# Kernel optimization log

Measured on AMD Instinct MI355X. Metric: run time of the kernel, lower is better.

Reference implementation:

```python
import jax, jax.numpy as jnp
import numpy as np

D = 2048
N = 16384
E = 8
THRESHOLD = 0.5


def setup_inputs() -> dict:
    key = jax.random.key(0)
    ks = jax.random.split(key, 6)
    x = jax.random.normal(ks[0], (N, D), dtype=jnp.float32)
    # pretrained weight + truncated SVD basis (frozen in original module)
    W_np = np.asarray(jax.random.normal(ks[1], (D, D), dtype=jnp.float32))
    U, S, Vt = np.linalg.svd(W_np, full_matrices=False)
    k = int((np.cumsum(S) < THRESHOLD * S.sum()).sum())  # energy-threshold rank
    U_k = jnp.asarray(U[:, :k])
    V_k = jnp.asarray(Vt.T[:, :k])  # torch.svd returns V, not V^T
    W = jnp.asarray(W_np)
    lambda_k = jax.random.normal(ks[2], (E, k), dtype=jnp.float32)
    v = jnp.zeros((D,), dtype=jnp.float32)
    W_g1 = jax.random.normal(ks[3], (k, 1), dtype=jnp.float32)
    W_g2 = jax.random.normal(ks[4], (1, E), dtype=jnp.float32)
    return {"x": x, "W": W, "U_k": U_k, "V_k": V_k, "lambda_k": lambda_k,
            "v": v, "W_g1": W_g1, "W_g2": W_g2}


def reference(x, W, U_k, V_k, lambda_k, v, W_g1, W_g2):
    # Routing: g = softmax((x @ U_k) @ W_g1 @ W_g2)  -> [N, E]
    xu = x @ U_k                                   # [N, k] (shared with delta path)
    g = jax.nn.softmax((xu @ W_g1) @ W_g2, axis=-1)
    # sum_i g_i * (x @ (W + U diag(lam_i) V^T))
    #   = (x@W) * sum_i g_i  +  ((x@U) * (g @ lam)) @ V^T   (low-rank factored)
    base = x @ W                                   # [N, D], computed once
    coef = g @ lambda_k                            # [N, k]
    out = base * jnp.sum(g, axis=-1, keepdims=True) + (xu * coef) @ V_k.T
    return out * (1.0 + v)
```

## Files before the change

kernel.cpp:

```cpp
#include <hip/hip_runtime.h>
#include <hip/hip_bf16.h>

#define D_DIM 2048
#define E_DIM 8

typedef __attribute__((ext_vector_type(8))) short short8;
typedef __attribute__((ext_vector_type(4))) float f32x4;

__device__ __forceinline__ unsigned short f2bf(float f) {
  union { float f; unsigned int u; } v; v.f = f;
  unsigned int u = v.u;
  u += 0x7FFFu + ((u >> 16) & 1u);
  return (unsigned short)(u >> 16);
}

__device__ __forceinline__ void async_copy16(const void* g, void* l) {
  __builtin_amdgcn_global_load_lds((const __attribute__((address_space(1))) void*)g,
                                   (__attribute__((address_space(3))) void*)l,
                                   16, 0, 0);
}

__global__ void k_cvt_bf16(const float* __restrict__ in,
                           unsigned short* __restrict__ out, long long n) {
  long long i = ((long long)blockIdx.x * blockDim.x + threadIdx.x) * 8;
  const long long stride = (long long)gridDim.x * blockDim.x * 8;
  for (; i < n; i += stride) {
    float4 a = *(const float4*)(in + i);
    float4 b = *(const float4*)(in + i + 4);
    short8 r;
    r[0] = (short)f2bf(a.x); r[1] = (short)f2bf(a.y);
    r[2] = (short)f2bf(a.z); r[3] = (short)f2bf(a.w);
    r[4] = (short)f2bf(b.x); r[5] = (short)f2bf(b.y);
    r[6] = (short)f2bf(b.z); r[7] = (short)f2bf(b.w);
    *(short8*)(out + i) = r;
  }
}

__global__ void k_transpose_bf16(const float* __restrict__ in, int in_rows, int in_cols,
                                 int in_ld, unsigned short* __restrict__ out, int out_rows) {
  __shared__ float tile[32][33];
  const int tx = threadIdx.x;
  const int ty = threadIdx.y;
  const int c = blockIdx.x * 32 + tx;
  #pragma unroll
  for (int i = 0; i < 4; ++i) {
    const int r = blockIdx.y * 32 + ty + i * 8;
    float vv = 0.0f;
    if (r < in_rows && c < in_cols) vv = in[(size_t)r * in_ld + c];
    tile[ty + i * 8][tx] = vv;
  }
  __syncthreads();
  const int oc = blockIdx.y * 32 + tx;
  #pragma unroll
  for (int i = 0; i < 4; ++i) {
    const int orow = blockIdx.x * 32 + ty + i * 8;
    if (orow < out_rows && oc < in_rows)
      out[(size_t)orow * in_rows + oc] = f2bf(tile[tx][ty + i * 8]);
  }
}

__global__ void k_pad_bf16(const float* __restrict__ in, unsigned short* __restrict__ out,
                           int rows, int cols, int cols_pad) {
  long long idx = (long long)blockIdx.x * blockDim.x + threadIdx.x;
  const long long total = (long long)rows * cols_pad;
  const long long stride = (long long)gridDim.x * blockDim.x;
  for (; idx < total; idx += stride) {
    const int r = (int)(idx / cols_pad);
    const int c = (int)(idx % cols_pad);
    out[idx] = (c < cols) ? f2bf(in[(size_t)r * cols + c]) : (unsigned short)0;
  }
}

__global__ void k_route(const float* __restrict__ xu, int k, int k_pad,
                        const float* __restrict__ Wg1, const float* __restrict__ Wg2,
                        const float* __restrict__ lam,
                        unsigned short* __restrict__ A2, float* __restrict__ rowscale,
                        int Nrows) {
  const int w = threadIdx.x >> 6;
  const int lane = threadIdx.x & 63;
  const int row = blockIdx.x * 4 + w;
  if (row >= Nrows) return;
  const float* xr = xu + (size_t)row * k_pad;
  float s = 0.0f;
  for (int kk = lane; kk < k; kk += 64) s += xr[kk] * Wg1[kk];
  #pragma unroll
  for (int off = 32; off; off >>= 1) s += __shfl_xor(s, off);
  float lg[E_DIM];
  float mx = -INFINITY;
  #pragma unroll
  for (int e = 0; e < E_DIM; ++e) { lg[e] = s * Wg2[e]; mx = fmaxf(mx, lg[e]); }
  float Z = 0.0f;
  #pragma unroll
  for (int e = 0; e < E_DIM; ++e) { lg[e] = expf(lg[e] - mx); Z += lg[e]; }
  float g[E_DIM]; float gsum = 0.0f;
  #pragma unroll
  for (int e = 0; e < E_DIM; ++e) { g[e] = lg[e] / Z; gsum += g[e]; }
  const float inv = 1.0f / gsum;
  if (lane == 0) rowscale[row] = gsum;
  unsigned short* arow = A2 + (size_t)row * k_pad;
  for (int kk = lane; kk < k_pad; kk += 64) {
    if (kk < k) {
      float c = 0.0f;
      #pragma unroll
      for (int e = 0; e < E_DIM; ++e) c += g[e] * lam[(size_t)e * k + kk];
      arow[kk] = f2bf(xr[kk] * (c * inv));
    } else {
      arow[kk] = 0;
    }
  }
}

__global__ __launch_bounds__(256, 2) void k_gemm128(
    const unsigned short* __restrict__ A, long long lda,
    const unsigned short* __restrict__ B, long long ldb,
    int Ktot, float* __restrict__ Cout, int ldc) {
  __shared__ unsigned short lds[4 * 8192];
  const int tid = threadIdx.x;
  const int lane = tid & 63;
  const int w = tid >> 6;
  const long long brow = (long long)blockIdx.x * 128;
  const long long bcol = (long long)blockIdx.y * 128;
  const int c0 = w * 2;
  const int sr0 = lane >> 2;
  const int sj  = lane & 3;
  const int l15 = lane & 15;
  const int jhi = lane >> 4;
  const int wr = (w >> 1) * 64;
  const int wc = (w & 1) * 64;

  auto stage = [&](int tt) {
    unsigned short* dstA = lds + (tt & 3) * 8192;
    #pragma unroll
    for (int c = 0; c < 2; ++c) {
      const int chunk = c0 + c;
      const int lrow = chunk * 16 + sr0;
      const int jj = sj ^ ((lrow >> 1) & 3);
      async_copy16(A + (brow + lrow) * lda + (long long)tt * 32 + jj * 8,
                   (void*)(dstA + chunk * 512));
      async_copy16(B + (bcol + lrow) * ldb + (long long)tt * 32 + jj * 8,
                   (void*)(dstA + 4096 + chunk * 512));
    }
  };

  auto load_frags = [&](int tt, short8* av, short8* bv) {
    const unsigned short* Areg = lds + (tt & 3) * 8192;
    const unsigned short* Breg = Areg + 4096;
    #pragma unroll
    for (int m = 0; m < 4; ++m) {
      const int row = wr + m * 16 + l15;
      const int jj = jhi ^ ((row >> 1) & 3);
      av[m] = *(const short8*)(Areg + row * 32 + jj * 8);
    }
    #pragma unroll
    for (int n = 0; n < 4; ++n) {
      const int row = wc + n * 16 + l15;
      const int jj = jhi ^ ((row >> 1) & 3);
      bv[n] = *(const short8*)(Breg + row * 32 + jj * 8);
    }
  };

  f32x4 acc[4][4];
  #pragma unroll
  for (int m = 0; m < 4; ++m)
    #pragma unroll
    for (int n = 0; n < 4; ++n)
      #pragma unroll
      for (int j = 0; j < 4; ++j) acc[m][n][j] = 0.0f;

  auto do_mfma = [&](short8* av, short8* bv) {
    __builtin_amdgcn_s_setprio(1);
    #pragma unroll
    for (int m = 0; m < 4; ++m)
      #pragma unroll
      for (int n = 0; n < 4; ++n)
        acc[m][n] = __builtin_amdgcn_mfma_f32_16x16x32_bf16(av[m], bv[n], acc[m][n], 0, 0, 0);
    __builtin_amdgcn_s_setprio(0);
  };

  const int NT = Ktot >> 5;
  stage(0); stage(1); stage(2);
  asm volatile("s_waitcnt vmcnt(4)" ::: "memory");
  __builtin_amdgcn_s_barrier();

  short8 avA[4], bvA[4], avB[4], bvB[4];
  load_frags(0, avA, bvA);

  for (int t = 0; t < NT; t += 2) {
    if (t + 3 < NT) stage(t + 3);
    load_frags(t + 1, avB, bvB);
    do_mfma(avA, bvA);
    asm volatile("s_waitcnt vmcnt(4)" ::: "memory");
    __builtin_amdgcn_s_barrier();
    if (t + 4 < NT) stage(t + 4);
    if (t + 2 < NT) load_frags(t + 2, avA, bvA);
    do_mfma(avB, bvB);
    asm volatile("s_waitcnt vmcnt(4)" ::: "memory");
    __builtin_amdgcn_s_barrier();
  }

  #pragma unroll
  for (int m = 0; m < 4; ++m) {
    #pragma unroll
    for (int n = 0; n < 4; ++n) {
      const long long col = bcol + wc + n * 16 + l15;
      #pragma unroll
      for (int j = 0; j < 4; ++j) {
        const long long row = brow + wr + m * 16 + jhi * 4 + j;
        Cout[row * ldc + col] = acc[m][n][j];
      }
    }
  }
}

template<int EPI>
__global__ __launch_bounds__(512, 2) void k_gemm256(
    const unsigned short* __restrict__ A0, int lda0,
    const unsigned short* __restrict__ A1, int lda1,
    const unsigned short* __restrict__ B0, int ldb0,
    const unsigned short* __restrict__ B1, int ldb1,
    int ka0, int Ktot, int gridM,
    float* __restrict__ Cout, int ldc,
    const float* __restrict__ rowscale, const float* __restrict__ vcol) {
  __shared__ unsigned short lds[4 * 16384];
  const int tid = threadIdx.x;
  const int lane = tid & 63;
  const int w = tid >> 6;
  const int wm = w >> 2;
  const int wn = w & 3;

  int bid = blockIdx.x;
  const int cpx = gridDim.x >> 3;
  bid = (bid & 7) * cpx + (bid >> 3);
  const int bx = bid % gridM;
  const int by = bid / gridM;
  const long long brow = (long long)bx * 256;
  const long long bcol = (long long)by * 256;

  const int c0 = w * 2;
  const int sr0 = lane >> 2;
  const int sj  = lane & 3;
  const int l15 = lane & 15;
  const int jhi = lane >> 4;

  auto stage = [&](int tt) {
    const int k0 = tt * 32;
    const unsigned short* PA; long long ldA; long long kA;
    const unsigned short* PB; long long ldB; long long kB;
    if (k0 < ka0) { PA = A0; ldA = lda0; kA = k0;       PB = B0; ldB = ldb0; kB = k0; }
    else          { PA = A1; ldA = lda1; kA = k0 - ka0; PB = B1; ldB = ldb1; kB = k0 - ka0; }
    unsigned short* dst = lds + (tt & 3) * 16384;
    #pragma unroll
    for (int c = 0; c < 2; ++c) {
      const int chunk = c0 + c;
      const int lrow = chunk * 16 + sr0;
      const int jj = sj ^ ((lrow >> 1) & 3);
      async_copy16(PA + (brow + lrow) * ldA + kA + jj * 8, (void*)(dst + chunk * 512));
      async_copy16(PB + (bcol + lrow) * ldB + kB + jj * 8, (void*)(dst + 8192 + chunk * 512));
    }
  };

  auto load_frags = [&](int tt, short8* av, short8* bv) {
    const unsigned short* Areg = lds + (tt & 3) * 16384;
    const unsigned short* Breg = Areg + 8192;
    #pragma unroll
    for (int m = 0; m < 8; ++m) {
      const int row = wm * 128 + m * 16 + l15;
      const int jj = jhi ^ ((row >> 1) & 3);
      av[m] = *(const short8*)(Areg + row * 32 + jj * 8);
    }
    #pragma unroll
    for (int n = 0; n < 4; ++n) {
      const int row = wn * 64 + n * 16 + l15;
      const int jj = jhi ^ ((row >> 1) & 3);
      bv[n] = *(const short8*)(Breg + row * 32 + jj * 8);
    }
  };

  f32x4 acc[8][4];
  #pragma unroll
  for (int m = 0; m < 8; ++m)
    #pragma unroll
    for (int n = 0; n < 4; ++n)
      #pragma unroll
      for (int j = 0; j < 4; ++j) acc[m][n][j] = 0.0f;

  auto do_mfma = [&](short8* av, short8* bv) {
    __builtin_amdgcn_s_setprio(1);
    #pragma unroll
    for (int m = 0; m < 8; ++m)
      #pragma unroll
      for (int n = 0; n < 4; ++n)
        acc[m][n] = __builtin_amdgcn_mfma_f32_16x16x32_bf16(av[m], bv[n], acc[m][n], 0, 0, 0);
    __builtin_amdgcn_s_setprio(0);
  };

  const int NT = Ktot >> 5;
  stage(0); stage(1); stage(2);
  asm volatile("s_waitcnt vmcnt(4)" ::: "memory");
  __builtin_amdgcn_s_barrier();

  short8 avA[8], bvA[4], avB[8], bvB[4];
  load_frags(0, avA, bvA);

  for (int t = 0; t < NT; t += 2) {
    if (t + 3 < NT) stage(t + 3);
    load_frags(t + 1, avB, bvB);
    do_mfma(avA, bvA);
    asm volatile("s_waitcnt vmcnt(4)" ::: "memory");
    __builtin_amdgcn_s_barrier();
    if (t + 4 < NT) stage(t + 4);
    if (t + 2 < NT) load_frags(t + 2, avA, bvA);
    do_mfma(avB, bvB);
    asm volatile("s_waitcnt vmcnt(4)" ::: "memory");
    __builtin_amdgcn_s_barrier();
  }

  #pragma unroll
  for (int m = 0; m < 8; ++m) {
    #pragma unroll
    for (int n = 0; n < 4; ++n) {
      const long long col = bcol + wn * 64 + n * 16 + l15;
      float cs = 1.0f;
      if (EPI == 1) cs = 1.0f + vcol[col];
      #pragma unroll
      for (int j = 0; j < 4; ++j) {
        const long long row = brow + wm * 128 + m * 16 + jhi * 4 + j;
        float val = acc[m][n][j];
        if (EPI == 1) val *= rowscale[row] * cs;
        Cout[row * ldc + col] = val;
      }
    }
  }
}

extern "C" void kernel_launch(void* const* d_in, const int* in_sizes, int n_in,
                              void* d_out, int out_size, void* d_ws, size_t ws_size,
                              hipStream_t stream) {
  const float* x   = (const float*)d_in[0];
  const float* W   = (const float*)d_in[1];
  const float* U   = (const float*)d_in[2];
  const float* V   = (const float*)d_in[3];
  const float* lam = (const float*)d_in[4];
  const float* v   = (const float*)d_in[5];
  const float* Wg1 = (const float*)d_in[6];
  const float* Wg2 = (const float*)d_in[7];
  float* out = (float*)d_out;

  const int N = in_sizes[0] / D_DIM;
  const int k = in_sizes[2] / D_DIM;
  const int k_pad = (k + 127) & ~127;

  char* ws = (char*)d_ws;
  size_t off = 0;
  auto alloc = [&](size_t bytes) -> void* {
    void* p = ws + off;
    off += (bytes + 255) & ~(size_t)255;
    return p;
  };
  unsigned short* xb  = (unsigned short*)alloc((size_t)N * D_DIM * 2);
  unsigned short* Wt  = (unsigned short*)alloc((size_t)D_DIM * D_DIM * 2);
  unsigned short* Ukt = (unsigned short*)alloc((size_t)k_pad * D_DIM * 2);
  unsigned short* Vb  = (unsigned short*)alloc((size_t)D_DIM * k_pad * 2);
  float*          xu  = (float*)alloc((size_t)N * k_pad * 4);
  unsigned short* A2  = (unsigned short*)alloc((size_t)N * k_pad * 2);
  float*          rs  = (float*)alloc((size_t)N * 4);
  if (off > ws_size) return;

  k_cvt_bf16<<<2048, 256, 0, stream>>>(x, xb, (long long)N * D_DIM);
  k_transpose_bf16<<<dim3(D_DIM / 32, D_DIM / 32), dim3(32, 8), 0, stream>>>(
      W, D_DIM, D_DIM, D_DIM, Wt, D_DIM);
  k_transpose_bf16<<<dim3(k_pad / 32, D_DIM / 32), dim3(32, 8), 0, stream>>>(
      U, D_DIM, k, k, Ukt, k_pad);
  k_pad_bf16<<<512, 256, 0, stream>>>(V, Vb, D_DIM, k, k_pad);

  k_gemm128<<<dim3(N / 128, k_pad / 128), 256, 0, stream>>>(
      xb, D_DIM, Ukt, D_DIM, D_DIM, xu, k_pad);

  k_route<<<N / 4, 256, 0, stream>>>(xu, k, k_pad, Wg1, Wg2, lam, A2, rs, N);

  const int gridM = N / 256;
  const int gridN = D_DIM / 256;
  k_gemm256<1><<<gridM * gridN, 512, 0, stream>>>(
      xb, D_DIM, A2, k_pad,
      Wt, D_DIM, Vb, k_pad,
      D_DIM, D_DIM + k_pad, gridM,
      out, D_DIM, rs, v);
}
```

Before: 344.4 us.

## Restructure GEMM main loop into split-phase A/B staging with per-half MFMA

Splits the global-to-LDS staging into separate A and B halves and interleaves them with two half-tile MFMA phases per K step, replacing the double-buffered register fragments with a single smaller set. This cuts register pressure and is meant to overlap memory issue with compute more finely, following a ping-pong style schedule. In exchange it adds extra barriers per iteration and tail-dependent vmcnt waits, which may serialize waves and risks correctness if the wait counts do not match the outstanding loads.

```diff
diff --git a/kernel.cpp b/kernel.cpp
--- a/kernel.cpp
+++ b/kernel.cpp
@@ -242,12 +242,11 @@
   const int l15 = lane & 15;
   const int jhi = lane >> 4;
 
-  auto stage = [&](int tt) {
+  auto stageA = [&](int tt) {
     const int k0 = tt * 32;
     const unsigned short* PA; long long ldA; long long kA;
-    const unsigned short* PB; long long ldB; long long kB;
-    if (k0 < ka0) { PA = A0; ldA = lda0; kA = k0;       PB = B0; ldB = ldb0; kB = k0; }
-    else          { PA = A1; ldA = lda1; kA = k0 - ka0; PB = B1; ldB = ldb1; kB = k0 - ka0; }
+    if (k0 < ka0) { PA = A0; ldA = lda0; kA = k0; }
+    else          { PA = A1; ldA = lda1; kA = k0 - ka0; }
     unsigned short* dst = lds + (tt & 3) * 16384;
     #pragma unroll
     for (int c = 0; c < 2; ++c) {
@@ -255,15 +254,43 @@
       const int lrow = chunk * 16 + sr0;
       const int jj = sj ^ ((lrow >> 1) & 3);
       async_copy16(PA + (brow + lrow) * ldA + kA + jj * 8, (void*)(dst + chunk * 512));
-      async_copy16(PB + (bcol + lrow) * ldB + kB + jj * 8, (void*)(dst + 8192 + chunk * 512));
-    }
-  };
-
-  auto load_frags = [&](int tt, short8* av, short8* bv) {
-    const unsigned short* Areg = lds + (tt & 3) * 16384;
+    }
+  };
+  auto stageB = [&](int tt) {
+    const int k0 = tt * 32;
+    const unsigned short* PB; long long ldB; long long kB;
+    if (k0 < ka0) { PB = B0; ldB = ldb0; kB = k0; }
+    else          { PB = B1; ldB = ldb1; kB = k0 - ka0; }
+    unsigned short* dst = lds + (tt & 3) * 16384 + 8192;
+    #pragma unroll
+    for (int c = 0; c < 2; ++c) {
+      const int chunk = c0 + c;
+      const int lrow = chunk * 16 + sr0;
+      const int jj = sj ^ ((lrow >> 1) & 3);
+      async_copy16(PB + (bcol + lrow) * ldB + kB + jj * 8, (void*)(dst + chunk * 512));
+    }
+  };
+
+  f32x4 acc[8][4];
+  #pragma unroll
+  for (int m = 0; m < 8; ++m)
+    #pragma unroll
+    for (int n = 0; n < 4; ++n)
+      #pragma unroll
+      for (int j = 0; j < 4; ++j) acc[m][n][j] = 0.0f;
+
+  const int NT = Ktot >> 5;
+  for (int p = 0; p < 3; ++p) { stageA(p); stageB(p); }
+  asm volatile("s_waitcnt vmcnt(8)" ::: "memory");
+  __builtin_amdgcn_s_barrier();
+
+  for (int t = 0; t < NT; ++t) {
+    const unsigned short* Areg = lds + (t & 3) * 16384;
     const unsigned short* Breg = Areg + 8192;
-    #pragma unroll
-    for (int m = 0; m < 8; ++m) {
+    short8 av[4], bv[4];
+
+    #pragma unroll
+    for (int m = 0; m < 4; ++m) {
       const int row = wm * 128 + m * 16 + l15;
       const int jj = jhi ^ ((row >> 1) & 3);
       av[m] = *(const short8*)(Areg + row * 32 + jj * 8);
@@ -274,44 +301,37 @@
       const int jj = jhi ^ ((row >> 1) & 3);
       bv[n] = *(const short8*)(Breg + row * 32 + jj * 8);
     }
-  };
-
-  f32x4 acc[8][4];
-  #pragma unroll
-  for (int m = 0; m < 8; ++m)
-    #pragma unroll
-    for (int n = 0; n < 4; ++n)
-      #pragma unroll
-      for (int j = 0; j < 4; ++j) acc[m][n][j] = 0.0f;
-
-  auto do_mfma = [&](short8* av, short8* bv) {
+    if (t + 3 < NT) stageA(t + 3);
+    __builtin_amdgcn_s_barrier();
+    asm volatile("s_waitcnt lgkmcnt(0)" ::: "memory");
     __builtin_amdgcn_s_setprio(1);
     #pragma unroll
-    for (int m = 0; m < 8; ++m)
+    for (int m = 0; m < 4; ++m)
       #pragma unroll
       for (int n = 0; n < 4; ++n)
         acc[m][n] = __builtin_amdgcn_mfma_f32_16x16x32_bf16(av[m], bv[n], acc[m][n], 0, 0, 0);
     __builtin_amdgcn_s_setprio(0);
-  };
-
-  const int NT = Ktot >> 5;
-  stage(0); stage(1); stage(2);
-  asm volatile("s_waitcnt vmcnt(4)" ::: "memory");
-  __builtin_amdgcn_s_barrier();
-
-  short8 avA[8], bvA[4], avB[8], bvB[4];
-  load_frags(0, avA, bvA);
-
-  for (int t = 0; t < NT; t += 2) {
-    if (t + 3 < NT) stage(t + 3);
-    load_frags(t + 1, avB, bvB);
-    do_mfma(avA, bvA);
-    asm volatile("s_waitcnt vmcnt(4)" ::: "memory");
-    __builtin_amdgcn_s_barrier();
-    if (t + 4 < NT) stage(t + 4);
-    if (t + 2 < NT) load_frags(t + 2, avA, bvA);
-    do_mfma(avB, bvB);
-    asm volatile("s_waitcnt vmcnt(4)" ::: "memory");
+    __builtin_amdgcn_s_barrier();
+
+    #pragma unroll
+    for (int m = 0; m < 4; ++m) {
+      const int row = wm * 128 + (4 + m) * 16 + l15;
+      const int jj = jhi ^ ((row >> 1) & 3);
+      av[m] = *(const short8*)(Areg + row * 32 + jj * 8);
+    }
+    if (t + 3 < NT) stageB(t + 3);
+    __builtin_amdgcn_s_barrier();
+    asm volatile("s_waitcnt lgkmcnt(0)" ::: "memory");
+    __builtin_amdgcn_s_setprio(1);
+    #pragma unroll
+    for (int m = 0; m < 4; ++m)
+      #pragma unroll
+      for (int n = 0; n < 4; ++n)
+        acc[4 + m][n] = __builtin_amdgcn_mfma_f32_16x16x32_bf16(av[m], bv[n], acc[4 + m][n], 0, 0, 0);
+    __builtin_amdgcn_s_setprio(0);
+    if (t + 3 < NT)      asm volatile("s_waitcnt vmcnt(8)" ::: "memory");
+    else if (t + 2 < NT) asm volatile("s_waitcnt vmcnt(4)" ::: "memory");
+    else if (t + 1 < NT) asm volatile("s_waitcnt vmcnt(0)" ::: "memory");
     __builtin_amdgcn_s_barrier();
   }
 
```

After: 361.2 us. 4.9% more time.

## Concatenate A/B operands into single buffers and precompute LDS/global addresses

Applied to the files above, without the earlier changes.

Writes x in bf16 and the routed low-rank activations side by side in one concatenated A buffer, and W^T with padded V in one concatenated B buffer. The main GEMM then streams a single operand pair and no longer branches per k-tile between two sources. Both GEMMs now precompute LDS fragment offsets and global pointers, and unroll the pipeline by four so the buffer slots are compile-time constants. The block-to-tile swizzle is also changed. The cost is wider row strides (D+k_pad) in the buffers.

```diff
diff --git a/kernel.cpp b/kernel.cpp
--- a/kernel.cpp
+++ b/kernel.cpp
@@ -20,24 +20,31 @@
                                    16, 0, 0);
 }
 
-__global__ void k_cvt_bf16(const float* __restrict__ in,
-                           unsigned short* __restrict__ out, long long n) {
-  long long i = ((long long)blockIdx.x * blockDim.x + threadIdx.x) * 8;
-  const long long stride = (long long)gridDim.x * blockDim.x * 8;
-  for (; i < n; i += stride) {
-    float4 a = *(const float4*)(in + i);
-    float4 b = *(const float4*)(in + i + 4);
-    short8 r;
-    r[0] = (short)f2bf(a.x); r[1] = (short)f2bf(a.y);
-    r[2] = (short)f2bf(a.z); r[3] = (short)f2bf(a.w);
-    r[4] = (short)f2bf(b.x); r[5] = (short)f2bf(b.y);
-    r[6] = (short)f2bf(b.z); r[7] = (short)f2bf(b.w);
-    *(short8*)(out + i) = r;
+__global__ void k_cvt_bf16s(const float* __restrict__ in,
+                            unsigned short* __restrict__ out,
+                            int rows, int cols, int out_ld) {
+  const int cpr = cols >> 3;
+  long long i = (long long)blockIdx.x * blockDim.x + threadIdx.x;
+  const long long total = (long long)rows * cpr;
+  const long long stride = (long long)gridDim.x * blockDim.x;
+  for (; i < total; i += stride) {
+    const int r = (int)(i / cpr);
+    const int c8 = (int)(i % cpr);
+    const float* src = in + (size_t)r * cols + c8 * 8;
+    float4 a = *(const float4*)(src);
+    float4 b = *(const float4*)(src + 4);
+    short8 rr;
+    rr[0] = (short)f2bf(a.x); rr[1] = (short)f2bf(a.y);
+    rr[2] = (short)f2bf(a.z); rr[3] = (short)f2bf(a.w);
+    rr[4] = (short)f2bf(b.x); rr[5] = (short)f2bf(b.y);
+    rr[6] = (short)f2bf(b.z); rr[7] = (short)f2bf(b.w);
+    *(short8*)(out + (size_t)r * out_ld + c8 * 8) = rr;
   }
 }
 
 __global__ void k_transpose_bf16(const float* __restrict__ in, int in_rows, int in_cols,
-                                 int in_ld, unsigned short* __restrict__ out, int out_rows) {
+                                 int in_ld, unsigned short* __restrict__ out,
+                                 int out_rows, int out_ld) {
   __shared__ float tile[32][33];
   const int tx = threadIdx.x;
   const int ty = threadIdx.y;
@@ -55,27 +62,28 @@
   for (int i = 0; i < 4; ++i) {
     const int orow = blockIdx.x * 32 + ty + i * 8;
     if (orow < out_rows && oc < in_rows)
-      out[(size_t)orow * in_rows + oc] = f2bf(tile[tx][ty + i * 8]);
+      out[(size_t)orow * out_ld + oc] = f2bf(tile[tx][ty + i * 8]);
   }
 }
 
 __global__ void k_pad_bf16(const float* __restrict__ in, unsigned short* __restrict__ out,
-                           int rows, int cols, int cols_pad) {
+                           int rows, int cols, int cols_pad, int out_ld) {
   long long idx = (long long)blockIdx.x * blockDim.x + threadIdx.x;
   const long long total = (long long)rows * cols_pad;
   const long long stride = (long long)gridDim.x * blockDim.x;
   for (; idx < total; idx += stride) {
     const int r = (int)(idx / cols_pad);
     const int c = (int)(idx % cols_pad);
-    out[idx] = (c < cols) ? f2bf(in[(size_t)r * cols + c]) : (unsigned short)0;
+    out[(size_t)r * out_ld + c] = (c < cols) ? f2bf(in[(size_t)r * cols + c])
+                                             : (unsigned short)0;
   }
 }
 
 __global__ void k_route(const float* __restrict__ xu, int k, int k_pad,
                         const float* __restrict__ Wg1, const float* __restrict__ Wg2,
                         const float* __restrict__ lam,
-                        unsigned short* __restrict__ A2, float* __restrict__ rowscale,
-                        int Nrows) {
+                        unsigned short* __restrict__ Acat, int acat_ld,
+                        float* __restrict__ rowscale, int Nrows) {
   const int w = threadIdx.x >> 6;
   const int lane = threadIdx.x & 63;
   const int row = blockIdx.x * 4 + w;
@@ -97,7 +105,7 @@
   for (int e = 0; e < E_DIM; ++e) { g[e] = lg[e] / Z; gsum += g[e]; }
   const float inv = 1.0f / gsum;
   if (lane == 0) rowscale[row] = gsum;
-  unsigned short* arow = A2 + (size_t)row * k_pad;
+  unsigned short* arow = Acat + (size_t)row * acat_ld + D_DIM;
   for (int kk = lane; kk < k_pad; kk += 64) {
     if (kk < k) {
       float c = 0.0f;
@@ -111,53 +119,39 @@
 }
 
 __global__ __launch_bounds__(256, 2) void k_gemm128(
-    const unsigned short* __restrict__ A, long long lda,
-    const unsigned short* __restrict__ B, long long ldb,
+    const unsigned short* __restrict__ A, int lda,
+    const unsigned short* __restrict__ B, int ldb,
     int Ktot, float* __restrict__ Cout, int ldc) {
-  __shared__ unsigned short lds[4 * 8192];
+  __shared__ unsigned short lds[32768];
+  char* ldsc = (char*)lds;
   const int tid = threadIdx.x;
   const int lane = tid & 63;
   const int w = tid >> 6;
   const long long brow = (long long)blockIdx.x * 128;
   const long long bcol = (long long)blockIdx.y * 128;
   const int c0 = w * 2;
-  const int sr0 = lane >> 2;
-  const int sj  = lane & 3;
-  const int l15 = lane & 15;
-  const int jhi = lane >> 4;
+  const int sr0 = lane >> 2, sj = lane & 3;
+  const int l15 = lane & 15, jhi = lane >> 4;
+  const int jx = jhi ^ ((l15 >> 1) & 3);
+  const int sjx = sj ^ ((sr0 >> 1) & 3);
   const int wr = (w >> 1) * 64;
   const int wc = (w & 1) * 64;
 
-  auto stage = [&](int tt) {
-    unsigned short* dstA = lds + (tt & 3) * 8192;
-    #pragma unroll
-    for (int c = 0; c < 2; ++c) {
-      const int chunk = c0 + c;
-      const int lrow = chunk * 16 + sr0;
-      const int jj = sj ^ ((lrow >> 1) & 3);
-      async_copy16(A + (brow + lrow) * lda + (long long)tt * 32 + jj * 8,
-                   (void*)(dstA + chunk * 512));
-      async_copy16(B + (bcol + lrow) * ldb + (long long)tt * 32 + jj * 8,
-                   (void*)(dstA + 4096 + chunk * 512));
-    }
-  };
-
-  auto load_frags = [&](int tt, short8* av, short8* bv) {
-    const unsigned short* Areg = lds + (tt & 3) * 8192;
-    const unsigned short* Breg = Areg + 4096;
-    #pragma unroll
-    for (int m = 0; m < 4; ++m) {
-      const int row = wr + m * 16 + l15;
-      const int jj = jhi ^ ((row >> 1) & 3);
-      av[m] = *(const short8*)(Areg + row * 32 + jj * 8);
-    }
-    #pragma unroll
-    for (int n = 0; n < 4; ++n) {
-      const int row = wc + n * 16 + l15;
-      const int jj = jhi ^ ((row >> 1) & 3);
-      bv[n] = *(const short8*)(Breg + row * 32 + jj * 8);
-    }
-  };
+  int preA[4], preB[4];
+  #pragma unroll
+  for (int m = 0; m < 4; ++m) preA[m] = ((w >> 1) * 4 + m) * 4096 + l15 * 64 + jx * 16;
+  #pragma unroll
+  for (int n = 0; n < 4; ++n) preB[n] = 32768 + ((w & 1) * 4 + n) * 4096 + l15 * 64 + jx * 16;
+
+  const char* gA[2]; const char* gB[2]; char* dA[2]; char* dB[2];
+  #pragma unroll
+  for (int cc = 0; cc < 2; ++cc) {
+    const int ch = c0 + cc;
+    gA[cc] = (const char*)A + ((brow + ch * 16 + sr0) * (long long)lda + sjx * 8) * 2;
+    gB[cc] = (const char*)B + ((bcol + ch * 16 + sr0) * (long long)ldb + sjx * 8) * 2;
+    dA[cc] = ldsc + ch * 4096;
+    dB[cc] = ldsc + 32768 + ch * 4096;
+  }
 
   f32x4 acc[4][4];
   #pragma unroll
@@ -165,9 +159,15 @@
     #pragma unroll
     for (int n = 0; n < 4; ++n)
       #pragma unroll
-      for (int j = 0; j < 4; ++j) acc[m][n][j] = 0.0f;
-
-  auto do_mfma = [&](short8* av, short8* bv) {
+      for (int q = 0; q < 4; ++q) acc[m][n][q] = 0.0f;
+
+  auto LOADF = [&](int S, short8* av, short8* bv) {
+    #pragma unroll
+    for (int m = 0; m < 4; ++m) av[m] = *(const short8*)(ldsc + (preA[m] + S * 1024));
+    #pragma unroll
+    for (int n = 0; n < 4; ++n) bv[n] = *(const short8*)(ldsc + (preB[n] + S * 1024));
+  };
+  auto MF = [&](short8* av, short8* bv) {
     __builtin_amdgcn_s_setprio(1);
     #pragma unroll
     for (int m = 0; m < 4; ++m)
@@ -178,24 +178,38 @@
   };
 
   const int NT = Ktot >> 5;
-  stage(0); stage(1); stage(2);
+  #pragma unroll
+  for (int p = 0; p < 3; ++p)
+    #pragma unroll
+    for (int cc = 0; cc < 2; ++cc) {
+      async_copy16(gA[cc] + p * 64, dA[cc] + p * 1024);
+      async_copy16(gB[cc] + p * 64, dB[cc] + p * 1024);
+    }
   asm volatile("s_waitcnt vmcnt(4)" ::: "memory");
   __builtin_amdgcn_s_barrier();
 
   short8 avA[4], bvA[4], avB[4], bvB[4];
-  load_frags(0, avA, bvA);
-
-  for (int t = 0; t < NT; t += 2) {
-    if (t + 3 < NT) stage(t + 3);
-    load_frags(t + 1, avB, bvB);
-    do_mfma(avA, bvA);
-    asm volatile("s_waitcnt vmcnt(4)" ::: "memory");
-    __builtin_amdgcn_s_barrier();
-    if (t + 4 < NT) stage(t + 4);
-    if (t + 2 < NT) load_frags(t + 2, avA, bvA);
-    do_mfma(avB, bvB);
-    asm volatile("s_waitcnt vmcnt(4)" ::: "memory");
-    __builtin_amdgcn_s_barrier();
+  LOADF(0, avA, bvA);
+
+  for (int tg = 0; tg < NT; tg += 4) {
+    #pragma unroll
+    for (int T4 = 0; T4 < 4; ++T4) {
+      const int tt = tg + T4;
+      if (tt + 3 < NT) {
+        const int S = (T4 + 3) & 3;
+        #pragma unroll
+        for (int cc = 0; cc < 2; ++cc) {
+          async_copy16(gA[cc] + (T4 + 3) * 64, dA[cc] + S * 1024);
+          async_copy16(gB[cc] + (T4 + 3) * 64, dB[cc] + S * 1024);
+        }
+      }
+      if ((T4 & 1) == 0) { LOADF((T4 + 1) & 3, avB, bvB); MF(avA, bvA); }
+      else               { LOADF((T4 + 1) & 3, avA, bvA); MF(avB, bvB); }
+      asm volatile("s_waitcnt vmcnt(4)" ::: "memory");
+      __builtin_amdgcn_s_barrier();
+    }
+    #pragma unroll
+    for (int cc = 0; cc < 2; ++cc) { gA[cc] += 256; gB[cc] += 256; }
   }
 
   #pragma unroll
@@ -204,9 +218,9 @@
     for (int n = 0; n < 4; ++n) {
       const long long col = bcol + wc + n * 16 + l15;
       #pragma unroll
-      for (int j = 0; j < 4; ++j) {
-        const long long row = brow + wr + m * 16 + jhi * 4 + j;
-        Cout[row * ldc + col] = acc[m][n][j];
+      for (int q = 0; q < 4; ++q) {
+        const long long row = brow + wr + m * 16 + jhi * 4 + q;
+        Cout[row * ldc + col] = acc[m][n][q];
       }
     }
   }
@@ -214,67 +228,47 @@
 
 template<int EPI>
 __global__ __launch_bounds__(512, 2) void k_gemm256(
-    const unsigned short* __restrict__ A0, int lda0,
-    const unsigned short* __restrict__ A1, int lda1,
-    const unsigned short* __restrict__ B0, int ldb0,
-    const unsigned short* __restrict__ B1, int ldb1,
-    int ka0, int Ktot, int gridM,
+    const unsigned short* __restrict__ A, int lda,
+    const unsigned short* __restrict__ B, int ldb,
+    int Ktot, int nx, int ny,
     float* __restrict__ Cout, int ldc,
     const float* __restrict__ rowscale, const float* __restrict__ vcol) {
-  __shared__ unsigned short lds[4 * 16384];
+  __shared__ unsigned short lds[65536];
+  char* ldsc = (char*)lds;
   const int tid = threadIdx.x;
   const int lane = tid & 63;
   const int w = tid >> 6;
-  const int wm = w >> 2;
-  const int wn = w & 3;
-
-  int bid = blockIdx.x;
-  const int cpx = gridDim.x >> 3;
-  bid = (bid & 7) * cpx + (bid >> 3);
-  const int bx = bid % gridM;
-  const int by = bid / gridM;
+  const int wm = w >> 2, wn = w & 3;
+
+  const int bid = blockIdx.x;
+  const int x = bid & 7;
+  const int j = bid >> 3;
+  const int bx = x * (nx >> 3) + j / ny;
+  const int by = j % ny;
   const long long brow = (long long)bx * 256;
   const long long bcol = (long long)by * 256;
 
   const int c0 = w * 2;
-  const int sr0 = lane >> 2;
-  const int sj  = lane & 3;
-  const int l15 = lane & 15;
-  const int jhi = lane >> 4;
-
-  auto stage = [&](int tt) {
-    const int k0 = tt * 32;
-    const unsigned short* PA; long long ldA; long long kA;
-    const unsigned short* PB; long long ldB; long long kB;
-    if (k0 < ka0) { PA = A0; ldA = lda0; kA = k0;       PB = B0; ldB = ldb0; kB = k0; }
-    else          { PA = A1; ldA = lda1; kA = k0 - ka0; PB = B1; ldB = ldb1; kB = k0 - ka0; }
-    unsigned short* dst = lds + (tt & 3) * 16384;
-    #pragma unroll
-    for (int c = 0; c < 2; ++c) {
-      const int chunk = c0 + c;
-      const int lrow = chunk * 16 + sr0;
-      const int jj = sj ^ ((lrow >> 1) & 3);
-      async_copy16(PA + (brow + lrow) * ldA + kA + jj * 8, (void*)(dst + chunk * 512));
-      async_copy16(PB + (bcol + lrow) * ldB + kB + jj * 8, (void*)(dst + 8192 + chunk * 512));
-    }
-  };
-
-  auto load_frags = [&](int tt, short8* av, short8* bv) {
-    const unsigned short* Areg = lds + (tt & 3) * 16384;
-    const unsigned short* Breg = Areg + 8192;
-    #pragma unroll
-    for (int m = 0; m < 8; ++m) {
-      const int row = wm * 128 + m * 16 + l15;
-      const int jj = jhi ^ ((row >> 1) & 3);
-      av[m] = *(const short8*)(Areg + row * 32 + jj * 8);
-    }
-    #pragma unroll
-    for (int n = 0; n < 4; ++n) {
-      const int row = wn * 64 + n * 16 + l15;
-      const int jj = jhi ^ ((row >> 1) & 3);
-      bv[n] = *(const short8*)(Breg + row * 32 + jj * 8);
-    }
-  };
+  const int sr0 = lane >> 2, sj = lane & 3;
+  const int l15 = lane & 15, jhi = lane >> 4;
+  const int jx = jhi ^ ((l15 >> 1) & 3);
+  const int sjx = sj ^ ((sr0 >> 1) & 3);
+
+  int preA[8], preB[4];
+  #pragma unroll
+  for (int m = 0; m < 8; ++m) preA[m] = (wm * 8 + m) * 4096 + l15 * 64 + jx * 16;
+  #pragma unroll
+  for (int n = 0; n < 4; ++n) preB[n] = 65536 + (wn * 4 + n) * 4096 + l15 * 64 + jx * 16;
+
+  const char* gA[2]; const char* gB[2]; char* dA[2]; char* dB[2];
+  #pragma unroll
+  for (int cc = 0; cc < 2; ++cc) {
+    const int ch = c0 + cc;
+    gA[cc] = (const char*)A + ((brow + ch * 16 + sr0) * (long long)lda + sjx * 8) * 2;
+    gB[cc] = (const char*)B + ((bcol + ch * 16 + sr0) * (long long)ldb + sjx * 8) * 2;
+    dA[cc] = ldsc + ch * 4096;
+    dB[cc] = ldsc + 65536 + ch * 4096;
+  }
 
   f32x4 acc[8][4];
   #pragma unroll
@@ -282,9 +276,15 @@
     #pragma unroll
     for (int n = 0; n < 4; ++n)
       #pragma unroll
-      for (int j = 0; j < 4; ++j) acc[m][n][j] = 0.0f;
-
-  auto do_mfma = [&](short8* av, short8* bv) {
+      for (int q = 0; q < 4; ++q) acc[m][n][q] = 0.0f;
+
+  auto LOADF = [&](int S, short8* av, short8* bv) {
+    #pragma unroll
+    for (int m = 0; m < 8; ++m) av[m] = *(const short8*)(ldsc + (preA[m] + S * 1024));
+    #pragma unroll
+    for (int n = 0; n < 4; ++n) bv[n] = *(const short8*)(ldsc + (preB[n] + S * 1024));
+  };
+  auto MF = [&](short8* av, short8* bv) {
     __builtin_amdgcn_s_setprio(1);
     #pragma unroll
     for (int m = 0; m < 8; ++m)
@@ -295,24 +295,38 @@
   };
 
   const int NT = Ktot >> 5;
-  stage(0); stage(1); stage(2);
+  #pragma unroll
+  for (int p = 0; p < 3; ++p)
+    #pragma unroll
+    for (int cc = 0; cc < 2; ++cc) {
+      async_copy16(gA[cc] + p * 64, dA[cc] + p * 1024);
+      async_copy16(gB[cc] + p * 64, dB[cc] + p * 1024);
+    }
   asm volatile("s_waitcnt vmcnt(4)" ::: "memory");
   __builtin_amdgcn_s_barrier();
 
   short8 avA[8], bvA[4], avB[8], bvB[4];
-  load_frags(0, avA, bvA);
-
-  for (int t = 0; t < NT; t += 2) {
-    if (t + 3 < NT) stage(t + 3);
-    load_frags(t + 1, avB, bvB);
-    do_mfma(avA, bvA);
-    asm volatile("s_waitcnt vmcnt(4)" ::: "memory");
-    __builtin_amdgcn_s_barrier();
-    if (t + 4 < NT) stage(t + 4);
-    if (t + 2 < NT) load_frags(t + 2, avA, bvA);
-    do_mfma(avB, bvB);
-    asm volatile("s_waitcnt vmcnt(4)" ::: "memory");
-    __builtin_amdgcn_s_barrier();
+  LOADF(0, avA, bvA);
+
+  for (int tg = 0; tg < NT; tg += 4) {
+    #pragma unroll
+    for (int T4 = 0; T4 < 4; ++T4) {
+      const int tt = tg + T4;
+      if (tt + 3 < NT) {
+        const int S = (T4 + 3) & 3;
+        #pragma unroll
+        for (int cc = 0; cc < 2; ++cc) {
+          async_copy16(gA[cc] + (T4 + 3) * 64, dA[cc] + S * 1024);
+          async_copy16(gB[cc] + (T4 + 3) * 64, dB[cc] + S * 1024);
+        }
+      }
+      if ((T4 & 1) == 0) { LOADF((T4 + 1) & 3, avB, bvB); MF(avA, bvA); }
+      else               { LOADF((T4 + 1) & 3, avA, bvA); MF(avB, bvB); }
+      asm volatile("s_waitcnt vmcnt(4)" ::: "memory");
+      __builtin_amdgcn_s_barrier();
+    }
+    #pragma unroll
+    for (int cc = 0; cc < 2; ++cc) { gA[cc] += 256; gB[cc] += 256; }
   }
 
   #pragma unroll
@@ -323,9 +337,9 @@
       float cs = 1.0f;
       if (EPI == 1) cs = 1.0f + vcol[col];
       #pragma unroll
-      for (int j = 0; j < 4; ++j) {
-        const long long row = brow + wm * 128 + m * 16 + jhi * 4 + j;
-        float val = acc[m][n][j];
+      for (int q = 0; q < 4; ++q) {
+        const long long row = brow + wm * 128 + m * 16 + jhi * 4 + q;
+        float val = acc[m][n][q];
         if (EPI == 1) val *= rowscale[row] * cs;
         Cout[row * ldc + col] = val;
       }
@@ -349,6 +363,7 @@
   const int N = in_sizes[0] / D_DIM;
   const int k = in_sizes[2] / D_DIM;
   const int k_pad = (k + 127) & ~127;
+  const int Ktot = D_DIM + k_pad;
 
   char* ws = (char*)d_ws;
   size_t off = 0;
@@ -357,32 +372,28 @@
     off += (bytes + 255) & ~(size_t)255;
     return p;
   };
-  unsigned short* xb  = (unsigned short*)alloc((size_t)N * D_DIM * 2);
-  unsigned short* Wt  = (unsigned short*)alloc((size_t)D_DIM * D_DIM * 2);
-  unsigned short* Ukt = (unsigned short*)alloc((size_t)k_pad * D_DIM * 2);
-  unsigned short* Vb  = (unsigned short*)alloc((size_t)D_DIM * k_pad * 2);
-  float*          xu  = (float*)alloc((size_t)N * k_pad * 4);
-  unsigned short* A2  = (unsigned short*)alloc((size_t)N * k_pad * 2);
-  float*          rs  = (float*)alloc((size_t)N * 4);
+  unsigned short* Acat = (unsigned short*)alloc((size_t)N * Ktot * 2);
+  unsigned short* Bcat = (unsigned short*)alloc((size_t)D_DIM * Ktot * 2);
+  unsigned short* Ukt  = (unsigned short*)alloc((size_t)k_pad * D_DIM * 2);
+  float*          xu   = (float*)alloc((size_t)N * k_pad * 4);
+  float*          rs   = (float*)alloc((size_t)N * 4);
   if (off > ws_size) return;
 
-  k_cvt_bf16<<<2048, 256, 0, stream>>>(x, xb, (long long)N * D_DIM);
+  k_cvt_bf16s<<<2048, 256, 0, stream>>>(x, Acat, N, D_DIM, Ktot);
   k_transpose_bf16<<<dim3(D_DIM / 32, D_DIM / 32), dim3(32, 8), 0, stream>>>(
-      W, D_DIM, D_DIM, D_DIM, Wt, D_DIM);
+      W, D_DIM, D_DIM, D_DIM, Bcat, D_DIM, Ktot);
   k_transpose_bf16<<<dim3(k_pad / 32, D_DIM / 32), dim3(32, 8), 0, stream>>>(
-      U, D_DIM, k, k, Ukt, k_pad);
-  k_pad_bf16<<<512, 256, 0, stream>>>(V, Vb, D_DIM, k, k_pad);
+      U, D_DIM, k, k, Ukt, k_pad, D_DIM);
+  k_pad_bf16<<<512, 256, 0, stream>>>(V, Bcat + D_DIM, D_DIM, k, k_pad, Ktot);
 
   k_gemm128<<<dim3(N / 128, k_pad / 128), 256, 0, stream>>>(
-      xb, D_DIM, Ukt, D_DIM, D_DIM, xu, k_pad);
-
-  k_route<<<N / 4, 256, 0, stream>>>(xu, k, k_pad, Wg1, Wg2, lam, A2, rs, N);
-
-  const int gridM = N / 256;
-  const int gridN = D_DIM / 256;
-  k_gemm256<1><<<gridM * gridN, 512, 0, stream>>>(
-      xb, D_DIM, A2, k_pad,
-      Wt, D_DIM, Vb, k_pad,
-      D_DIM, D_DIM + k_pad, gridM,
+      Acat, Ktot, Ukt, D_DIM, D_DIM, xu, k_pad);
+
+  k_route<<<N / 4, 256, 0, stream>>>(xu, k, k_pad, Wg1, Wg2, lam, Acat, Ktot, rs, N);
+
+  const int nx = N / 256;
+  const int ny = D_DIM / 256;
+  k_gemm256<1><<<nx * ny, 512, 0, stream>>>(
+      Acat, Ktot, Bcat, Ktot, Ktot, nx, ny,
       out, D_DIM, rs, v);
 }
```

New measurement: 492.0 us. +42.8%, slower.

## Replace 4-stage rotating LDS pipeline with double-buffered two-tile phases

Applied to the files above, without the earlier changes.

Reworks the 256x256 GEMM main loop from a 4-slot ring (3 tiles in flight, register-level fragment prefetch interleaved with MFMA) into a ping-pong scheme. Each phase stages two K-tiles into the alternate LDS half, loads both tiles' fragments, runs their MFMAs, then waits for all loads and syncs. This halves the number of barriers per K-step and simplifies the schedule. In exchange it loses the overlap of fragment loads with MFMA and only prefetches one phase ahead, so the full vmcnt(0) wait may expose more memory latency. There is also a possible LDS race: a phase issues async writes into the buffer that was read during the previous phase without a barrier between the last reads and the new writes.

```diff
diff --git a/kernel.cpp b/kernel.cpp
--- a/kernel.cpp
+++ b/kernel.cpp
@@ -221,7 +221,7 @@
     int ka0, int Ktot, int gridM,
     float* __restrict__ Cout, int ldc,
     const float* __restrict__ rowscale, const float* __restrict__ vcol) {
-  __shared__ unsigned short lds[4 * 16384];
+  __shared__ unsigned short lds[65536];
   const int tid = threadIdx.x;
   const int lane = tid & 63;
   const int w = tid >> 6;
@@ -242,31 +242,29 @@
   const int l15 = lane & 15;
   const int jhi = lane >> 4;
 
-  auto stage = [&](int tt) {
+  auto stage_tile = [&](int tt, unsigned short* base) {
     const int k0 = tt * 32;
     const unsigned short* PA; long long ldA; long long kA;
     const unsigned short* PB; long long ldB; long long kB;
     if (k0 < ka0) { PA = A0; ldA = lda0; kA = k0;       PB = B0; ldB = ldb0; kB = k0; }
     else          { PA = A1; ldA = lda1; kA = k0 - ka0; PB = B1; ldB = ldb1; kB = k0 - ka0; }
-    unsigned short* dst = lds + (tt & 3) * 16384;
     #pragma unroll
     for (int c = 0; c < 2; ++c) {
       const int chunk = c0 + c;
       const int lrow = chunk * 16 + sr0;
       const int jj = sj ^ ((lrow >> 1) & 3);
-      async_copy16(PA + (brow + lrow) * ldA + kA + jj * 8, (void*)(dst + chunk * 512));
-      async_copy16(PB + (bcol + lrow) * ldB + kB + jj * 8, (void*)(dst + 8192 + chunk * 512));
-    }
-  };
-
-  auto load_frags = [&](int tt, short8* av, short8* bv) {
-    const unsigned short* Areg = lds + (tt & 3) * 16384;
-    const unsigned short* Breg = Areg + 8192;
+      async_copy16(PA + (brow + lrow) * ldA + kA + jj * 8, (void*)(base + chunk * 512));
+      async_copy16(PB + (bcol + lrow) * ldB + kB + jj * 8, (void*)(base + 8192 + chunk * 512));
+    }
+  };
+
+  auto load_frags = [&](const unsigned short* base, short8* av, short8* bv) {
+    const unsigned short* Breg = base + 8192;
     #pragma unroll
     for (int m = 0; m < 8; ++m) {
       const int row = wm * 128 + m * 16 + l15;
       const int jj = jhi ^ ((row >> 1) & 3);
-      av[m] = *(const short8*)(Areg + row * 32 + jj * 8);
+      av[m] = *(const short8*)(base + row * 32 + jj * 8);
     }
     #pragma unroll
     for (int n = 0; n < 4; ++n) {
@@ -285,33 +283,37 @@
       for (int j = 0; j < 4; ++j) acc[m][n][j] = 0.0f;
 
   auto do_mfma = [&](short8* av, short8* bv) {
-    __builtin_amdgcn_s_setprio(1);
     #pragma unroll
     for (int m = 0; m < 8; ++m)
       #pragma unroll
       for (int n = 0; n < 4; ++n)
         acc[m][n] = __builtin_amdgcn_mfma_f32_16x16x32_bf16(av[m], bv[n], acc[m][n], 0, 0, 0);
+  };
+
+  const int NT = Ktot >> 5;
+  const int NP = NT >> 1;
+
+  stage_tile(0, lds);
+  stage_tile(1, lds + 16384);
+  asm volatile("s_waitcnt vmcnt(0)" ::: "memory");
+  __builtin_amdgcn_s_barrier();
+
+  short8 av0[8], bv0[4], av1[8], bv1[4];
+
+  for (int p = 0; p < NP; ++p) {
+    unsigned short* cur = lds + (p & 1) * 32768;
+    unsigned short* nxt = lds + ((p + 1) & 1) * 32768;
+    if (p + 1 < NP) {
+      stage_tile(2 * (p + 1),     nxt);
+      stage_tile(2 * (p + 1) + 1, nxt + 16384);
+    }
+    load_frags(cur,         av0, bv0);
+    load_frags(cur + 16384, av1, bv1);
+    __builtin_amdgcn_s_setprio(1);
+    do_mfma(av0, bv0);
+    do_mfma(av1, bv1);
     __builtin_amdgcn_s_setprio(0);
-  };
-
-  const int NT = Ktot >> 5;
-  stage(0); stage(1); stage(2);
-  asm volatile("s_waitcnt vmcnt(4)" ::: "memory");
-  __builtin_amdgcn_s_barrier();
-
-  short8 avA[8], bvA[4], avB[8], bvB[4];
-  load_frags(0, avA, bvA);
-
-  for (int t = 0; t < NT; t += 2) {
-    if (t + 3 < NT) stage(t + 3);
-    load_frags(t + 1, avB, bvB);
-    do_mfma(avA, bvA);
-    asm volatile("s_waitcnt vmcnt(4)" ::: "memory");
-    __builtin_amdgcn_s_barrier();
-    if (t + 4 < NT) stage(t + 4);
-    if (t + 2 < NT) load_frags(t + 2, avA, bvA);
-    do_mfma(avB, bvB);
-    asm volatile("s_waitcnt vmcnt(4)" ::: "memory");
+    asm volatile("s_waitcnt vmcnt(0)" ::: "memory");
     __builtin_amdgcn_s_barrier();
   }
 
```

New measurement: 352.9 us. 1.02x slower.
